# Performance work log

Measured on AMD Instinct MI355X. Metric: run time of the kernel, lower is better.

Reference implementation:

```python
import jax, jax.numpy as jnp
import numpy as np

NEG_SLOPE_GAT = 0.2   # PyG GATConv default negative_slope
NEG_SLOPE = 0.01      # torch.nn.LeakyReLU default
NUM_AISLES = 20       # aisle_nrs drawn from [0,20); matches aisle_nrs.max()+1


def leaky(x, s):
    return jnp.where(x >= 0, x, s * x)


def gat_conv(x, src, dst, W, a_src, a_dst, b, n_nodes):
    """Single-head PyG GATConv (self-loops already appended to src/dst)."""
    h = x @ W                                        # [N, C]
    es = h @ a_src                                   # [N]
    ed = h @ a_dst                                   # [N]
    e = leaky(es[src] + ed[dst], NEG_SLOPE_GAT)      # [E] per-edge score
    m = jax.ops.segment_max(e, dst, num_segments=n_nodes)
    w = jnp.exp(e - m[dst])
    z = jax.ops.segment_sum(w, dst, num_segments=n_nodes)
    alpha = w / z[dst]                               # segment softmax over incoming edges
    out = jax.ops.segment_sum(h[src] * alpha[:, None], dst, num_segments=n_nodes)
    return out + b


def setup_inputs() -> dict:
    key = jax.random.key(0)
    ks = jax.random.split(key, 32)
    B, N, E = 16, 2048, 32768
    Fin, H, O, HA = 32, 128, 64, 256

    def glorot(k, shape):
        fan = shape[0] + shape[-1]
        return jax.random.uniform(k, shape, jnp.float32, -1.0, 1.0) * np.sqrt(6.0 / fan)

    inp = {
        "graph_nodes": jax.random.normal(ks[0], (B, N, Fin), jnp.float32),
        "aisle_nrs": jax.random.randint(ks[1], (B, N), 0, NUM_AISLES),
        "graph_edge_links": jax.random.randint(ks[2], (B, 2, E), 0, N),
        "mask": jax.random.randint(ks[3], (B, N), 0, 2),
        "picks_left": jax.random.randint(ks[4], (B,), 0, 100),
        # GAT layer 1: Fin -> H
        "W1": glorot(ks[5], (Fin, H)), "as1": glorot(ks[6], (H,)), "ad1": glorot(ks[7], (H,)), "b1": jnp.zeros((H,), jnp.float32),
        # GAT layer 2: H -> H
        "W2": glorot(ks[8], (H, H)), "as2": glorot(ks[9], (H,)), "ad2": glorot(ks[10], (H,)), "b2": jnp.zeros((H,), jnp.float32),
        # GAT layer 3: H -> O
        "W3": glorot(ks[11], (H, O)), "as3": glorot(ks[12], (O,)), "ad3": glorot(ks[13], (O,)), "b3": jnp.zeros((O,), jnp.float32),
        # post-embedding MLP head
        "lw1": glorot(ks[14], (2 * O, HA)), "lb1": jnp.zeros((HA,), jnp.float32),
        "lw2": glorot(ks[15], (HA, O)), "lb2": jnp.zeros((O,), jnp.float32),
        "lw3": glorot(ks[16], (O, 1)), "lb3": jnp.zeros((1,), jnp.float32),
    }
    return inp


def reference(graph_nodes, aisle_nrs, graph_edge_links, mask, picks_left,
              W1, as1, ad1, b1, W2, as2, ad2, b2, W3, as3, ad3, b3,
              lw1, lb1, lw2, lb2, lw3, lb3):
    B, N, Fin = graph_nodes.shape
    NT = B * N
    x = graph_nodes.reshape(NT, Fin)

    # batch the graphs: offset per-graph edge indices, append self-loops
    off = (jnp.arange(B) * N)[:, None]
    src = (graph_edge_links[:, 0, :] + off).reshape(-1)
    dst = (graph_edge_links[:, 1, :] + off).reshape(-1)
    loops = jnp.arange(NT)
    src = jnp.concatenate([src, loops])
    dst = jnp.concatenate([dst, loops])

    x = gat_conv(x, src, dst, W1, as1, ad1, b1, NT)
    x = gat_conv(x, src, dst, W2, as2, ad2, b2, NT)
    x = gat_conv(x, src, dst, W3, as3, ad3, b3, NT)

    # scatter-mean aisle embedding
    batch_idx = jnp.repeat(jnp.arange(B), N)
    aid = aisle_nrs.reshape(-1) + batch_idx * NUM_AISLES   # [NT]
    S = B * NUM_AISLES
    ssum = jax.ops.segment_sum(x, aid, num_segments=S)
    cnt = jax.ops.segment_sum(jnp.ones((NT,), x.dtype), aid, num_segments=S)
    emb = ssum / jnp.maximum(cnt, 1.0)[:, None]

    x = jnp.concatenate([x, emb[aid]], axis=1)             # [NT, 2*O]
    x = leaky(x @ lw1 + lb1, NEG_SLOPE)
    x = leaky(x @ lw2 + lb2, NEG_SLOPE)
    x = (x @ lw3 + lb3).reshape(B, N)

    logits = jnp.where(mask != 0, x, -jnp.inf)
    return jax.nn.softmax(logits, axis=1)
```

## Files before the change

### kernel.cpp

```cpp
#include <hip/hip_runtime.h>
#include <hip/hip_bf16.h>
#include <math.h>

#define BATCH 16
#define NNODE 2048
#define EPG   32768
#define NT    (BATCH * NNODE)
#define ET    (BATCH * EPG + NT)
#define NUM_AISLES 20
#define SEG   (BATCH * NUM_AISLES)
#define NEG_GAT 0.2f
#define NEG_MLP 0.01f
#define ACHUNK 8
#define CAP 64

typedef __attribute__((ext_vector_type(8))) short s16x8;
typedef __attribute__((ext_vector_type(4))) float f32x4;

__device__ __forceinline__ void split_bf16(float v, unsigned short& hi, unsigned short& lo) {
    unsigned int u = __float_as_uint(v);
    unsigned int r = u + 0x7FFFu + ((u >> 16) & 1u);
    hi = (unsigned short)(r >> 16);
    float fh = __uint_as_float(((unsigned int)hi) << 16);
    float rem = v - fh;
    unsigned int u2 = __float_as_uint(rem);
    unsigned int r2 = u2 + 0x7FFFu + ((u2 >> 16) & 1u);
    lo = (unsigned short)(r2 >> 16);
}

__global__ __launch_bounds__(256) void edge_scatter(const int* __restrict__ links,
                                                    int* __restrict__ cnt,
                                                    int* __restrict__ col_bkt) {
    int b = blockIdx.x;
    int s, d;
    if (b < 2048) {
        int xcd = b & 7, idx = b >> 3;
        int g = xcd * 2 + (idx >> 7);
        int chunk = idx & 127;
        int i = chunk * 256 + threadIdx.x;
        const int* pb = links + (size_t)g * 2 * EPG;
        s = pb[i] + (g << 11);
        d = pb[EPG + i] + (g << 11);
    } else {
        int b2 = b - 2048;
        int xcd = b2 & 7, idx = b2 >> 3;
        int g = xcd * 2 + (idx >> 3);
        int chunk = idx & 7;
        s = d = g * NNODE + chunk * 256 + threadIdx.x;
    }
    int pos = atomicAdd(&cnt[d], 1);
    if (pos < CAP) col_bkt[d * CAP + pos] = s;
}

template <int K, int NOUT, int COLS, bool LEAKY, bool ATTN, bool FINAL, bool CONCAT>
__global__ __launch_bounds__(256) void gemm_mfma(const float* __restrict__ A,
                                                 const float* __restrict__ W,
                                                 const float* __restrict__ bias,
                                                 float* __restrict__ out,
                                                 const float* __restrict__ a_src,
                                                 const float* __restrict__ a_dst,
                                                 float* __restrict__ es,
                                                 float* __restrict__ ed,
                                                 const float* __restrict__ emb,
                                                 const int* __restrict__ aisle,
                                                 const float* __restrict__ lw3,
                                                 const float* __restrict__ lb3,
                                                 const int* __restrict__ mask,
                                                 float* __restrict__ logits) {
    constexpr int BM = 64;
    constexpr int C = COLS / 16;
    constexpr int LDA = 40;

    __shared__ unsigned short Ah[BM * LDA], Al[BM * LDA];
    __shared__ unsigned short Wh[COLS * LDA], Wl[COLS * LDA];

    const int tid = threadIdx.x;
    const int wave = tid >> 6, lane = tid & 63;
    const int quad = lane >> 4, l15 = lane & 15;
    const int row0 = blockIdx.x * BM;
    const int c0 = blockIdx.y * COLS;

    f32x4 acc[C];
#pragma unroll
    for (int c = 0; c < C; ++c)
#pragma unroll
        for (int v = 0; v < 4; ++v) acc[c][v] = 0.f;

    const int arow = tid >> 2;
    const int aq = tid & 3;

    for (int kc = 0; kc < K; kc += 32) {
        {
            const int node = row0 + arow;
            const int off = kc + aq * 8;
            const float* srcp;
            if constexpr (CONCAT) {
                if (off < 64) {
                    srcp = A + (size_t)node * 64 + off;
                } else {
                    int g = node >> 11;
                    srcp = emb + ((size_t)(g * NUM_AISLES + aisle[node])) * 64 + (off - 64);
                }
            } else {
                srcp = A + (size_t)node * K + off;
            }
            unsigned short* dh = Ah + arow * LDA + aq * 8;
            unsigned short* dl = Al + arow * LDA + aq * 8;
#pragma unroll
            for (int q = 0; q < 2; ++q) {
                float4 v = ((const float4*)srcp)[q];
                unsigned short h0, l0, h1, l1, h2, l2, h3, l3;
                split_bf16(v.x, h0, l0);
                split_bf16(v.y, h1, l1);
                split_bf16(v.z, h2, l2);
                split_bf16(v.w, h3, l3);
                dh[q * 4 + 0] = h0; dh[q * 4 + 1] = h1; dh[q * 4 + 2] = h2; dh[q * 4 + 3] = h3;
                dl[q * 4 + 0] = l0; dl[q * 4 + 1] = l1; dl[q * 4 + 2] = l2; dl[q * 4 + 3] = l3;
            }
        }
        for (int i = tid; i < 32 * COLS; i += 256) {
            int k = i / COLS;
            int n = i - k * COLS;
            unsigned short h, l;
            split_bf16(W[(size_t)(kc + k) * NOUT + c0 + n], h, l);
            Wh[n * LDA + k] = h;
            Wl[n * LDA + k] = l;
        }
        __syncthreads();
        {
            int m = wave * 16 + l15;
            s16x8 ah = *(const s16x8*)&Ah[m * LDA + quad * 8];
            s16x8 al = *(const s16x8*)&Al[m * LDA + quad * 8];
#pragma unroll
            for (int c = 0; c < C; ++c) {
                int n = c * 16 + l15;
                s16x8 wh = *(const s16x8*)&Wh[n * LDA + quad * 8];
                s16x8 wl = *(const s16x8*)&Wl[n * LDA + quad * 8];
                acc[c] = __builtin_amdgcn_mfma_f32_16x16x32_bf16(ah, wh, acc[c], 0, 0, 0);
                acc[c] = __builtin_amdgcn_mfma_f32_16x16x32_bf16(ah, wl, acc[c], 0, 0, 0);
                acc[c] = __builtin_amdgcn_mfma_f32_16x16x32_bf16(al, wh, acc[c], 0, 0, 0);
            }
        }
        __syncthreads();
    }
    if constexpr (FINAL) {
#pragma unroll
        for (int reg = 0; reg < 4; ++reg) {
            float p = 0.f;
#pragma unroll
            for (int c = 0; c < C; ++c) {
                int colx = c * 16 + l15;
                float v = acc[c][reg] + bias[colx];
                v = v >= 0.f ? v : NEG_MLP * v;
                p += v * lw3[colx];
            }
#pragma unroll
            for (int mk = 1; mk < 16; mk <<= 1) p += __shfl_xor(p, mk, 64);
            if (l15 == 0) {
                int row = row0 + wave * 16 + quad * 4 + reg;
                float lg = p + lb3[0];
                logits[row] = (mask[row] != 0) ? lg : -INFINITY;
            }
        }
    } else {
#pragma unroll
        for (int c = 0; c < C; ++c) {
            int colx = c0 + c * 16 + l15;
            float bv = bias ? bias[colx] : 0.f;
#pragma unroll
            for (int reg = 0; reg < 4; ++reg) {
                int row = row0 + wave * 16 + quad * 4 + reg;
                float v = acc[c][reg] + bv;
                if (LEAKY) v = v >= 0.f ? v : NEG_MLP * v;
                out[(size_t)row * NOUT + colx] = v;
            }
        }
        if constexpr (ATTN) {
#pragma unroll
            for (int reg = 0; reg < 4; ++reg) {
                float ps = 0.f, pd = 0.f;
#pragma unroll
                for (int c = 0; c < C; ++c) {
                    int colx = c * 16 + l15;
                    float v = acc[c][reg];
                    ps += v * a_src[colx];
                    pd += v * a_dst[colx];
                }
#pragma unroll
                for (int mk = 1; mk < 16; mk <<= 1) {
                    ps += __shfl_xor(ps, mk, 64);
                    pd += __shfl_xor(pd, mk, 64);
                }
                if (l15 == 0) {
                    int row = row0 + wave * 16 + quad * 4 + reg;
                    es[row] = ps;
                    ed[row] = pd;
                }
            }
        }
    }
}

template <int HD>
__global__ __launch_bounds__(256) void gat_aggregate(const float* __restrict__ h,
                                                     const float* __restrict__ es,
                                                     const float* __restrict__ ed,
                                                     const int* __restrict__ cnt,
                                                     const int* __restrict__ col_bkt,
                                                     const float* __restrict__ bias,
                                                     float* __restrict__ out) {
    int b = blockIdx.x;
    int xcd = b & 7, q = b >> 3;
    int graph = xcd * 2 + (q >> 9);
    int node = graph * NNODE + (q & 511) * 4 + (threadIdx.x >> 6);
    int lane = threadIdx.x & 63;
    int deg = cnt[node];
    deg = deg < CAP ? deg : CAP;
    float edv = ed[node];

    float e0 = -INFINITY;
    int c0v = 0;
    if (lane < deg) {
        c0v = col_bkt[node * CAP + lane];
        float e = es[c0v] + edv;
        e0 = e >= 0.f ? e : NEG_GAT * e;
    }
    float m = e0;
#pragma unroll
    for (int off = 32; off; off >>= 1) m = fmaxf(m, __shfl_xor(m, off, 64));
    float z = __expf(e0 - m);
#pragma unroll
    for (int off = 32; off; off >>= 1) z += __shfl_xor(z, off, 64);
    float w0 = __expf(e0 - m) / z;

    const int quad = lane >> 4, l15 = lane & 15;
    if (HD == 128) {
        float a0 = 0.f, a1 = 0.f, a2 = 0.f, a3 = 0.f;
        float a4 = 0.f, a5 = 0.f, a6 = 0.f, a7 = 0.f;
        for (int jj = 0; jj < deg; jj += 4) {
            int j2 = jj + quad;
            int s = __shfl(c0v, j2, 64);
            float w = __shfl(w0, j2, 64);
            const float* base = h + (size_t)s * 128 + l15 * 8;
            float4 v0 = *(const float4*)base;
            float4 v1 = *(const float4*)(base + 4);
            a0 += w * v0.x; a1 += w * v0.y; a2 += w * v0.z; a3 += w * v0.w;
            a4 += w * v1.x; a5 += w * v1.y; a6 += w * v1.z; a7 += w * v1.w;
        }
#pragma unroll
        for (int off = 16; off <= 32; off <<= 1) {
            a0 += __shfl_xor(a0, off, 64); a1 += __shfl_xor(a1, off, 64);
            a2 += __shfl_xor(a2, off, 64); a3 += __shfl_xor(a3, off, 64);
            a4 += __shfl_xor(a4, off, 64); a5 += __shfl_xor(a5, off, 64);
            a6 += __shfl_xor(a6, off, 64); a7 += __shfl_xor(a7, off, 64);
        }
        if (quad == 0) {
            const float* bb = bias + l15 * 8;
            float4 o0, o1;
            o0.x = a0 + bb[0]; o0.y = a1 + bb[1]; o0.z = a2 + bb[2]; o0.w = a3 + bb[3];
            o1.x = a4 + bb[4]; o1.y = a5 + bb[5]; o1.z = a6 + bb[6]; o1.w = a7 + bb[7];
            float* op = out + (size_t)node * 128 + l15 * 8;
            *(float4*)op = o0;
            *(float4*)(op + 4) = o1;
        }
    } else {
        float a0 = 0.f, a1 = 0.f, a2 = 0.f, a3 = 0.f;
        for (int jj = 0; jj < deg; jj += 4) {
            int j2 = jj + quad;
            int s = __shfl(c0v, j2, 64);
            float w = __shfl(w0, j2, 64);
            float4 v = *(const float4*)(h + (size_t)s * 64 + l15 * 4);
            a0 += w * v.x; a1 += w * v.y; a2 += w * v.z; a3 += w * v.w;
        }
#pragma unroll
        for (int off = 16; off <= 32; off <<= 1) {
            a0 += __shfl_xor(a0, off, 64); a1 += __shfl_xor(a1, off, 64);
            a2 += __shfl_xor(a2, off, 64); a3 += __shfl_xor(a3, off, 64);
        }
        if (quad == 0) {
            const float* bb = bias + l15 * 4;
            float4 o;
            o.x = a0 + bb[0]; o.y = a1 + bb[1]; o.z = a2 + bb[2]; o.w = a3 + bb[3];
            *(float4*)(out + (size_t)node * 64 + l15 * 4) = o;
        }
    }
}

__global__ __launch_bounds__(256) void aisle_partial(const float* __restrict__ x3,
                                                     const int* __restrict__ aisle,
                                                     float* __restrict__ psum,
                                                     int* __restrict__ pcnt) {
    int g = blockIdx.x >> 3;
    int ch = blockIdx.x & 7;
    int f = threadIdx.x & 63;
    int stripe = threadIdx.x >> 6;

    __shared__ float sacc[4][NUM_AISLES][64];
    __shared__ int scnt[4][NUM_AISLES];
    for (int i = threadIdx.x; i < 4 * NUM_AISLES * 64; i += 256)
        ((float*)sacc)[i] = 0.f;
    for (int i = threadIdx.x; i < 4 * NUM_AISLES; i += 256)
        ((int*)scnt)[i] = 0;
    __syncthreads();

    const int* ai = aisle + g * NNODE;
    const float* xg = x3 + (size_t)g * NNODE * 64;
    int n0 = ch * 256 + stripe * 64;
#pragma unroll 4
    for (int i = 0; i < 64; ++i) {
        int n = n0 + i;
        int a = ai[n];
        float v = xg[(size_t)n * 64 + f];
        sacc[stripe][a][f] += v;
        if (f == 0) scnt[stripe][a]++;
    }
    __syncthreads();

    for (int i = threadIdx.x; i < NUM_AISLES * 64; i += 256) {
        int a = i >> 6, ff = i & 63;
        psum[((size_t)blockIdx.x * NUM_AISLES + a) * 64 + ff] =
            sacc[0][a][ff] + sacc[1][a][ff] + sacc[2][a][ff] + sacc[3][a][ff];
    }
    for (int i = threadIdx.x; i < NUM_AISLES; i += 256) {
        pcnt[blockIdx.x * NUM_AISLES + i] =
            scnt[0][i] + scnt[1][i] + scnt[2][i] + scnt[3][i];
    }
}

__global__ __launch_bounds__(256) void aisle_reduce(const float* __restrict__ psum,
                                                    const int* __restrict__ pcnt,
                                                    float* __restrict__ emb) {
    int idx = blockIdx.x * 256 + threadIdx.x;
    if (idx >= SEG * 64) return;
    int seg = idx >> 6;
    int f = idx & 63;
    int g = seg / NUM_AISLES;
    int a = seg - g * NUM_AISLES;
    float s = 0.f;
    int c = 0;
#pragma unroll
    for (int ch = 0; ch < ACHUNK; ++ch) {
        int blk = g * ACHUNK + ch;
        s += psum[((size_t)blk * NUM_AISLES + a) * 64 + f];
        c += pcnt[blk * NUM_AISLES + a];
    }
    emb[idx] = s / fmaxf((float)c, 1.0f);
}

__global__ __launch_bounds__(256) void softmax_kernel(const float* __restrict__ logits,
                                                      float* __restrict__ out) {
    int b = blockIdx.x;
    const float* lr = logits + b * NNODE;
    __shared__ float red[4], redz[4];
    float m = -INFINITY;
    for (int i = threadIdx.x; i < NNODE; i += 256) m = fmaxf(m, lr[i]);
#pragma unroll
    for (int off = 32; off; off >>= 1) m = fmaxf(m, __shfl_xor(m, off, 64));
    if ((threadIdx.x & 63) == 0) red[threadIdx.x >> 6] = m;
    __syncthreads();
    m = fmaxf(fmaxf(red[0], red[1]), fmaxf(red[2], red[3]));
    float z = 0.f;
    for (int i = threadIdx.x; i < NNODE; i += 256) z += __expf(lr[i] - m);
#pragma unroll
    for (int off = 32; off; off >>= 1) z += __shfl_xor(z, off, 64);
    if ((threadIdx.x & 63) == 0) redz[threadIdx.x >> 6] = z;
    __syncthreads();
    z = redz[0] + redz[1] + redz[2] + redz[3];
    float invz = 1.0f / z;
    for (int i = threadIdx.x; i < NNODE; i += 256) {
        float v = lr[i];
        out[b * NNODE + i] = (v == -INFINITY) ? 0.f : __expf(v - m) * invz;
    }
}


extern "C" void kernel_launch(void* const* d_in, const int* in_sizes, int n_in,
                              void* d_out, int out_size, void* d_ws, size_t ws_size,
                              hipStream_t stream) {
    const float* gn   = (const float*)d_in[0];
    const int* aisle  = (const int*)d_in[1];
    const int* links  = (const int*)d_in[2];
    const int* mask   = (const int*)d_in[3];
    const float* W1  = (const float*)d_in[5];
    const float* as1 = (const float*)d_in[6];
    const float* ad1 = (const float*)d_in[7];
    const float* b1  = (const float*)d_in[8];
    const float* W2  = (const float*)d_in[9];
    const float* as2 = (const float*)d_in[10];
    const float* ad2 = (const float*)d_in[11];
    const float* b2  = (const float*)d_in[12];
    const float* W3  = (const float*)d_in[13];
    const float* as3 = (const float*)d_in[14];
    const float* ad3 = (const float*)d_in[15];
    const float* b3  = (const float*)d_in[16];
    const float* lw1 = (const float*)d_in[17];
    const float* lb1 = (const float*)d_in[18];
    const float* lw2 = (const float*)d_in[19];
    const float* lb2 = (const float*)d_in[20];
    const float* lw3 = (const float*)d_in[21];
    const float* lb3 = (const float*)d_in[22];
    float* out = (float*)d_out;

    float* ws = (float*)d_ws;
    float* h      = ws;
    float* xb     = h + (size_t)NT * 128;
    float* es     = xb + (size_t)NT * 128;
    float* ed     = es + NT;
    float* emb    = ed + NT;
    float* y1     = emb + SEG * 64;
    float* y2     = y1 + (size_t)NT * 256;
    float* logits = y2 + (size_t)NT * 64;
    float* psum   = logits + NT;
    int* pcnt     = (int*)(psum + 128 * NUM_AISLES * 64);
    int* row_ptr  = pcnt + 128 * NUM_AISLES;
    int* cnt      = row_ptr + NT + 1;
    int* col_bkt  = (int*)y2;

    const int EB = (ET + 255) / 256;

    hipMemsetAsync(cnt, 0, NT * sizeof(int), stream);
    edge_scatter<<<EB, 256, 0, stream>>>(links, cnt, col_bkt);

    gemm_mfma<32, 128, 128, false, true, false, false><<<dim3(NT / 64, 1), 256, 0, stream>>>(
        gn, W1, nullptr, h, as1, ad1, es, ed, nullptr, nullptr, nullptr, nullptr, nullptr, nullptr);
    gat_aggregate<128><<<NT / 4, 256, 0, stream>>>(h, es, ed, cnt, col_bkt, b1, xb);

    gemm_mfma<128, 128, 128, false, true, false, false><<<dim3(NT / 64, 1), 256, 0, stream>>>(
        xb, W2, nullptr, h, as2, ad2, es, ed, nullptr, nullptr, nullptr, nullptr, nullptr, nullptr);
    gat_aggregate<128><<<NT / 4, 256, 0, stream>>>(h, es, ed, cnt, col_bkt, b2, xb);

    gemm_mfma<128, 64, 64, false, true, false, false><<<dim3(NT / 64, 1), 256, 0, stream>>>(
        xb, W3, nullptr, h, as3, ad3, es, ed, nullptr, nullptr, nullptr, nullptr, nullptr, nullptr);
    gat_aggregate<64><<<NT / 4, 256, 0, stream>>>(h, es, ed, cnt, col_bkt, b3, xb);

    aisle_partial<<<BATCH * ACHUNK, 256, 0, stream>>>(xb, aisle, psum, pcnt);
    aisle_reduce<<<(SEG * 64 + 255) / 256, 256, 0, stream>>>(psum, pcnt, emb);

    gemm_mfma<128, 256, 128, true, false, false, true><<<dim3(NT / 64, 2), 256, 0, stream>>>(
        xb, lw1, lb1, y1, nullptr, nullptr, nullptr, nullptr, emb, aisle, nullptr, nullptr, nullptr, nullptr);
    gemm_mfma<256, 64, 64, true, false, true, false><<<dim3(NT / 64, 1), 256, 0, stream>>>(
        y1, lw2, lb2, y2, nullptr, nullptr, nullptr, nullptr, nullptr, nullptr, lw3, lb3, mask, logits);

    softmax_kernel<<<BATCH, 256, 0, stream>>>(logits, out);
}
```

Baseline: 325.2 us.

## Pre-split weights to bf16 hi/lo once and load MFMA operands directly from global

Adds a small kernel that converts all five weight matrices into transposed bf16 hi/lo arrays once per call. The GEMM kernel then drops its shared-memory staging and barriers: each lane loads and splits its own A fragment from global and reads its weight fragments straight from the pre-split arrays. This removes the repeated per-block weight splitting and the LDS round-trips and syncs. The cost is one extra launch, more uncoalesced global and L2 traffic for weight fragments, and A rows read with a strided per-lane pattern.

```diff
diff --git a/kernel.cpp b/kernel.cpp
--- a/kernel.cpp
+++ b/kernel.cpp
@@ -26,6 +26,38 @@
     unsigned int u2 = __float_as_uint(rem);
     unsigned int r2 = u2 + 0x7FFFu + ((u2 >> 16) & 1u);
     lo = (unsigned short)(r2 >> 16);
+}
+
+#define WT_W1  0
+#define WT_W2  4096
+#define WT_W3  20480
+#define WT_LW1 28672
+#define WT_LW2 61440
+#define WT_TOT 77824
+
+__global__ __launch_bounds__(256) void wsplit_kernel(const float* __restrict__ W1,
+                                                     const float* __restrict__ W2,
+                                                     const float* __restrict__ W3,
+                                                     const float* __restrict__ lw1,
+                                                     const float* __restrict__ lw2,
+                                                     unsigned short* __restrict__ wt_hi,
+                                                     unsigned short* __restrict__ wt_lo) {
+    int idx = blockIdx.x * 256 + threadIdx.x;
+    if (idx >= WT_TOT) return;
+    const float* src;
+    int base, K, N;
+    if (idx < WT_W2)      { src = W1;  base = WT_W1;  K = 32;  N = 128; }
+    else if (idx < WT_W3) { src = W2;  base = WT_W2;  K = 128; N = 128; }
+    else if (idx < WT_LW1){ src = W3;  base = WT_W3;  K = 128; N = 64;  }
+    else if (idx < WT_LW2){ src = lw1; base = WT_LW1; K = 128; N = 256; }
+    else                  { src = lw2; base = WT_LW2; K = 256; N = 64;  }
+    int local = idx - base;
+    int k = local / N;
+    int n = local - k * N;
+    unsigned short hi, lo;
+    split_bf16(src[(size_t)k * N + n], hi, lo);
+    wt_hi[base + (size_t)n * K + k] = hi;
+    wt_lo[base + (size_t)n * K + k] = lo;
 }
 
 __global__ __launch_bounds__(256) void edge_scatter(const int* __restrict__ links,
@@ -54,7 +86,8 @@
 
 template <int K, int NOUT, int COLS, bool LEAKY, bool ATTN, bool FINAL, bool CONCAT>
 __global__ __launch_bounds__(256) void gemm_mfma(const float* __restrict__ A,
-                                                 const float* __restrict__ W,
+                                                 const unsigned short* __restrict__ wt_hi,
+                                                 const unsigned short* __restrict__ wt_lo,
                                                  const float* __restrict__ bias,
                                                  float* __restrict__ out,
                                                  const float* __restrict__ a_src,
@@ -67,18 +100,14 @@
                                                  const float* __restrict__ lb3,
                                                  const int* __restrict__ mask,
                                                  float* __restrict__ logits) {
-    constexpr int BM = 64;
     constexpr int C = COLS / 16;
-    constexpr int LDA = 40;
-
-    __shared__ unsigned short Ah[BM * LDA], Al[BM * LDA];
-    __shared__ unsigned short Wh[COLS * LDA], Wl[COLS * LDA];
 
     const int tid = threadIdx.x;
     const int wave = tid >> 6, lane = tid & 63;
     const int quad = lane >> 4, l15 = lane & 15;
-    const int row0 = blockIdx.x * BM;
+    const int row0 = blockIdx.x * 64;
     const int c0 = blockIdx.y * COLS;
+    const int m = row0 + wave * 16 + l15;
 
     f32x4 acc[C];
 #pragma unroll
@@ -86,62 +115,37 @@
 #pragma unroll
         for (int v = 0; v < 4; ++v) acc[c][v] = 0.f;
 
-    const int arow = tid >> 2;
-    const int aq = tid & 3;
+    union SU { s16x8 v; unsigned short u[8]; };
 
     for (int kc = 0; kc < K; kc += 32) {
-        {
-            const int node = row0 + arow;
-            const int off = kc + aq * 8;
-            const float* srcp;
-            if constexpr (CONCAT) {
-                if (off < 64) {
-                    srcp = A + (size_t)node * 64 + off;
-                } else {
-                    int g = node >> 11;
-                    srcp = emb + ((size_t)(g * NUM_AISLES + aisle[node])) * 64 + (off - 64);
-                }
+        const int off = kc + quad * 8;
+        const float* srcp;
+        if constexpr (CONCAT) {
+            if (off < 64) {
+                srcp = A + (size_t)m * 64 + off;
             } else {
-                srcp = A + (size_t)node * K + off;
+                int g = m >> 11;
+                srcp = emb + ((size_t)(g * NUM_AISLES + aisle[m])) * 64 + (off - 64);
             }
-            unsigned short* dh = Ah + arow * LDA + aq * 8;
-            unsigned short* dl = Al + arow * LDA + aq * 8;
-#pragma unroll
-            for (int q = 0; q < 2; ++q) {
-                float4 v = ((const float4*)srcp)[q];
-                unsigned short h0, l0, h1, l1, h2, l2, h3, l3;
-                split_bf16(v.x, h0, l0);
-                split_bf16(v.y, h1, l1);
-                split_bf16(v.z, h2, l2);
-                split_bf16(v.w, h3, l3);
-                dh[q * 4 + 0] = h0; dh[q * 4 + 1] = h1; dh[q * 4 + 2] = h2; dh[q * 4 + 3] = h3;
-                dl[q * 4 + 0] = l0; dl[q * 4 + 1] = l1; dl[q * 4 + 2] = l2; dl[q * 4 + 3] = l3;
-            }
-        }
-        for (int i = tid; i < 32 * COLS; i += 256) {
-            int k = i / COLS;
-            int n = i - k * COLS;
-            unsigned short h, l;
-            split_bf16(W[(size_t)(kc + k) * NOUT + c0 + n], h, l);
-            Wh[n * LDA + k] = h;
-            Wl[n * LDA + k] = l;
-        }
-        __syncthreads();
-        {
-            int m = wave * 16 + l15;
-            s16x8 ah = *(const s16x8*)&Ah[m * LDA + quad * 8];
-            s16x8 al = *(const s16x8*)&Al[m * LDA + quad * 8];
-#pragma unroll
-            for (int c = 0; c < C; ++c) {
-                int n = c * 16 + l15;
-                s16x8 wh = *(const s16x8*)&Wh[n * LDA + quad * 8];
-                s16x8 wl = *(const s16x8*)&Wl[n * LDA + quad * 8];
-                acc[c] = __builtin_amdgcn_mfma_f32_16x16x32_bf16(ah, wh, acc[c], 0, 0, 0);
-                acc[c] = __builtin_amdgcn_mfma_f32_16x16x32_bf16(ah, wl, acc[c], 0, 0, 0);
-                acc[c] = __builtin_amdgcn_mfma_f32_16x16x32_bf16(al, wh, acc[c], 0, 0, 0);
-            }
-        }
-        __syncthreads();
+        } else {
+            srcp = A + (size_t)m * K + off;
+        }
+        float4 v0 = ((const float4*)srcp)[0];
+        float4 v1 = ((const float4*)srcp)[1];
+        float a8[8] = {v0.x, v0.y, v0.z, v0.w, v1.x, v1.y, v1.z, v1.w};
+        SU ah, al;
+#pragma unroll
+        for (int j = 0; j < 8; ++j) split_bf16(a8[j], ah.u[j], al.u[j]);
+
+#pragma unroll
+        for (int c = 0; c < C; ++c) {
+            size_t woff = (size_t)(c0 + c * 16 + l15) * K + kc + quad * 8;
+            s16x8 wh = *(const s16x8*)(wt_hi + woff);
+            s16x8 wl = *(const s16x8*)(wt_lo + woff);
+            acc[c] = __builtin_amdgcn_mfma_f32_16x16x32_bf16(ah.v, wh, acc[c], 0, 0, 0);
+            acc[c] = __builtin_amdgcn_mfma_f32_16x16x32_bf16(ah.v, wl, acc[c], 0, 0, 0);
+            acc[c] = __builtin_amdgcn_mfma_f32_16x16x32_bf16(al.v, wh, acc[c], 0, 0, 0);
+        }
     }
     if constexpr (FINAL) {
 #pragma unroll
@@ -415,31 +419,39 @@
     int* row_ptr  = pcnt + 128 * NUM_AISLES;
     int* cnt      = row_ptr + NT + 1;
     int* col_bkt  = (int*)y2;
+    unsigned short* wt_hi = (unsigned short*)(((uintptr_t)(cnt + NT) + 63) & ~(uintptr_t)63);
+    unsigned short* wt_lo = wt_hi + ((WT_TOT + 31) & ~31);
 
     const int EB = (ET + 255) / 256;
 
+    wsplit_kernel<<<(WT_TOT + 255) / 256, 256, 0, stream>>>(W1, W2, W3, lw1, lw2, wt_hi, wt_lo);
     hipMemsetAsync(cnt, 0, NT * sizeof(int), stream);
     edge_scatter<<<EB, 256, 0, stream>>>(links, cnt, col_bkt);
 
     gemm_mfma<32, 128, 128, false, true, false, false><<<dim3(NT / 64, 1), 256, 0, stream>>>(
-        gn, W1, nullptr, h, as1, ad1, es, ed, nullptr, nullptr, nullptr, nullptr, nullptr, nullptr);
+        gn, wt_hi + WT_W1, wt_lo + WT_W1, nullptr, h, as1, ad1, es, ed,
+        nullptr, nullptr, nullptr, nullptr, nullptr, nullptr);
     gat_aggregate<128><<<NT / 4, 256, 0, stream>>>(h, es, ed, cnt, col_bkt, b1, xb);
 
     gemm_mfma<128, 128, 128, false, true, false, false><<<dim3(NT / 64, 1), 256, 0, stream>>>(
-        xb, W2, nullptr, h, as2, ad2, es, ed, nullptr, nullptr, nullptr, nullptr, nullptr, nullptr);
+        xb, wt_hi + WT_W2, wt_lo + WT_W2, nullptr, h, as2, ad2, es, ed,
+        nullptr, nullptr, nullptr, nullptr, nullptr, nullptr);
     gat_aggregate<128><<<NT / 4, 256, 0, stream>>>(h, es, ed, cnt, col_bkt, b2, xb);
 
     gemm_mfma<128, 64, 64, false, true, false, false><<<dim3(NT / 64, 1), 256, 0, stream>>>(
-        xb, W3, nullptr, h, as3, ad3, es, ed, nullptr, nullptr, nullptr, nullptr, nullptr, nullptr);
+        xb, wt_hi + WT_W3, wt_lo + WT_W3, nullptr, h, as3, ad3, es, ed,
+        nullptr, nullptr, nullptr, nullptr, nullptr, nullptr);
     gat_aggregate<64><<<NT / 4, 256, 0, stream>>>(h, es, ed, cnt, col_bkt, b3, xb);
 
     aisle_partial<<<BATCH * ACHUNK, 256, 0, stream>>>(xb, aisle, psum, pcnt);
     aisle_reduce<<<(SEG * 64 + 255) / 256, 256, 0, stream>>>(psum, pcnt, emb);
 
     gemm_mfma<128, 256, 128, true, false, false, true><<<dim3(NT / 64, 2), 256, 0, stream>>>(
-        xb, lw1, lb1, y1, nullptr, nullptr, nullptr, nullptr, emb, aisle, nullptr, nullptr, nullptr, nullptr);
+        xb, wt_hi + WT_LW1, wt_lo + WT_LW1, lb1, y1, nullptr, nullptr, nullptr, nullptr,
+        emb, aisle, nullptr, nullptr, nullptr, nullptr);
     gemm_mfma<256, 64, 64, true, false, true, false><<<dim3(NT / 64, 1), 256, 0, stream>>>(
-        y1, lw2, lb2, y2, nullptr, nullptr, nullptr, nullptr, nullptr, nullptr, lw3, lb3, mask, logits);
+        y1, wt_hi + WT_LW2, wt_lo + WT_LW2, lb2, y2, nullptr, nullptr, nullptr, nullptr,
+        nullptr, nullptr, lw3, lb3, mask, logits);
 
     softmax_kernel<<<BATCH, 256, 0, stream>>>(logits, out);
 }
```

Result: slower. 340.7 us (+4.8%).
